# Performance work log

Measured on AMD Instinct MI355X. Metric: run time of the kernel, lower is better.

## Reference

```python
import jax, jax.numpy as jnp
import numpy as np


def setup_inputs() -> dict:
    key = jax.random.key(0)
    k_x, k_q, k_k, k_v = jax.random.split(key, 4)
    B, S, F, U = 8, 2048, 1024, 256
    x = jax.random.normal(k_x, (B, S, F), dtype=jnp.float32)
    Wq = jax.random.normal(k_q, (F, U), dtype=jnp.float32) * 0.05
    Wk = jax.random.normal(k_k, (F, U), dtype=jnp.float32) * 0.05
    Wv = jax.random.normal(k_v, (F, U), dtype=jnp.float32) * 0.05
    return {"x": x, "Wq": Wq, "Wk": Wk, "Wv": Wv}


def reference(x, Wq, Wk, Wv):
    # x: [B, S, F]; projections tanh-activated: [B, S, U]
    xQ = jnp.tanh(jnp.einsum("bsf,fu->bsu", x, Wq))
    xK = jnp.tanh(jnp.einsum("bsf,fu->bsu", x, Wk))
    xV = jnp.tanh(jnp.einsum("bsf,fu->bsu", x, Wv))
    scale = 1.0 / jnp.sqrt(jnp.asarray(x.shape[-1], dtype=jnp.float32))
    scores = jnp.einsum("bsu,btu->bst", xQ, xK) * scale  # [B, S, S]
    weights = jax.nn.softmax(scores, axis=-1)
    out = jnp.einsum("bst,btu->bsu", weights, xV)  # return_sequences=True
    return out
```

## Files before the change

kernel.cpp:

```cpp
#include <hip/hip_runtime.h>
#include <math.h>

#define B_ 8
#define S_ 2048
#define F_ 1024
#define U_ 256
#define M_ (B_ * S_)

typedef __attribute__((ext_vector_type(8))) short bf16x8;
typedef __attribute__((ext_vector_type(4))) float f32x4;
typedef __attribute__((ext_vector_type(16))) float f32x16;
typedef unsigned short ushort_t;

__device__ __forceinline__ unsigned short f2bf(float x) {
    unsigned u = __builtin_bit_cast(unsigned, x);
    unsigned r = (u + 0x7fffu + ((u >> 16) & 1u)) >> 16;
    return (unsigned short)r;
}
__device__ __forceinline__ float bf2f(unsigned short b) {
    return __builtin_bit_cast(float, ((unsigned)b) << 16);
}
__device__ __forceinline__ void gload16(const void* g, void* l) {
    __builtin_amdgcn_global_load_lds(
        (const __attribute__((address_space(1))) unsigned int*)g,
        (__attribute__((address_space(3))) unsigned int*)l, 16, 0, 0);
}
__device__ __forceinline__ f32x4 zero4() {
    f32x4 v; v[0] = 0.f; v[1] = 0.f; v[2] = 0.f; v[3] = 0.f; return v;
}

__global__ __launch_bounds__(256) void convxt_kernel(
    const float* __restrict__ x, ushort_t* __restrict__ xbt)
{
    __shared__ ushort_t T[8][129][8];

    const int t  = threadIdx.x;
    const int r0 = blockIdx.x * 128;
    const int k0 = blockIdx.y * 64;

    #pragma unroll
    for (int i = 0; i < 8; ++i) {
        const int r = i * 16 + (t >> 4);
        const int c = (t & 15) * 4;
        const float4 v = *reinterpret_cast<const float4*>(
            x + (size_t)(r0 + r) * F_ + k0 + c);
        ushort4 o;
        o.x = f2bf(v.x); o.y = f2bf(v.y); o.z = f2bf(v.z); o.w = f2bf(v.w);
        *reinterpret_cast<ushort4*>(&T[c >> 3][r][c & 7]) = o;
    }
    __syncthreads();
    #pragma unroll
    for (int i = 0; i < 4; ++i) {
        const int ci  = i * 256 + t;
        const int ksl = ci >> 7, r = ci & 127;
        ushort_t* dst = xbt + ((size_t)(blockIdx.y * 8 + ksl) * M_ + r0 + r) * 8;
        *reinterpret_cast<bf16x8*>(dst) =
            *reinterpret_cast<const bf16x8*>(&T[ksl][r][0]);
    }
}

__global__ __launch_bounds__(256) void convw_kernel(
    const float* __restrict__ Wq, const float* __restrict__ Wk,
    const float* __restrict__ Wv, ushort_t* __restrict__ Wp)
{
    const int ks   = blockIdx.x;
    const int wsel = blockIdx.y;
    const float* __restrict__ W = (wsel == 0) ? Wq : (wsel == 1) ? Wk : Wv;
    const int n = threadIdx.x;

    bf16x8 hv, lv;
    #pragma unroll
    for (int j = 0; j < 8; ++j) {
        float v = W[(size_t)(ks * 8 + j) * U_ + n];
        ushort_t h = f2bf(v);
        hv[j] = (short)h;
        lv[j] = (short)f2bf(v - bf2f(h));
    }
    size_t base = (size_t)wsel * 524288;
    *reinterpret_cast<bf16x8*>(&Wp[base + ((size_t)ks) * 2048 + n * 8]) = hv;
    *reinterpret_cast<bf16x8*>(&Wp[base + ((size_t)(128 + ks)) * 2048 + n * 8]) = lv;
}

__global__ __launch_bounds__(256, 3) void proj_mfma_kernel(
    const ushort_t* __restrict__ xbt,
    const ushort_t* __restrict__ Wp,
    ushort_t* __restrict__ qh_g, ushort_t* __restrict__ kh_g,
    ushort_t* __restrict__ vth_g)
{
    __shared__ ushort_t As[2][4 * 128 * 8];
    __shared__ ushort_t Bs[2][2 * 4 * 128 * 8];

    const int orig = blockIdx.x;
    const int xcd  = orig & 7;
    const int i    = orig >> 3;
    const int rt6  = i / 6;
    const int sub  = i - rt6 * 6;
    const int wsel = sub >> 1;
    const int nh   = sub & 1;
    const int row0 = (xcd * 16 + rt6) * 128;
    const int col0 = nh * 128;
    const bool twopass = (wsel == 2);

    const int tid = threadIdx.x;
    const int l = tid & 63, w = tid >> 6;
    const int wy = w >> 1, wx = w & 1;
    const int m = l & 31, hi = l >> 5;

    const ushort_t* __restrict__ WpB = Wp + (size_t)wsel * 524288;

    f32x16 acc[2][2];
    #pragma unroll
    for (int mr = 0; mr < 2; ++mr)
        #pragma unroll
        for (int nf = 0; nf < 2; ++nf)
            #pragma unroll
            for (int r = 0; r < 16; ++r) acc[mr][nf][r] = 0.f;

    auto stageA = [&](int buf, int ks) {
        #pragma unroll
        for (int it = 0; it < 2; ++it) {
            const int ci = it * 256 + tid;
            const int ksl = ci >> 7, r = ci & 127;
            const ushort_t* src =
                xbt + ((size_t)(ks * 4 + ksl) * M_ + row0 + r) * 8;
            gload16(src, (char*)&As[buf][0] + (size_t)(it * 256 + w * 64) * 16);
        }
    };
    auto stageB = [&](int buf, int ks) {
        const int nit = twopass ? 4 : 2;
        for (int it = 0; it < nit; ++it) {
            const int ci = it * 256 + tid;
            const int half = ci >> 9, ksl = (ci >> 7) & 3, n = ci & 127;
            const ushort_t* src = WpB + (size_t)half * 262144
                                  + (size_t)(ks * 4 + ksl) * 2048
                                  + (size_t)(col0 + n) * 8;
            gload16(src, (char*)&Bs[buf][0] + (size_t)(it * 256 + w * 64) * 16);
        }
    };

    stageA(0, 0);
    stageB(0, 0);
    __syncthreads();

    for (int ks = 0; ks < 32; ++ks) {
        const int cur = ks & 1;
        if (ks < 31) { stageA(cur ^ 1, ks + 1); stageB(cur ^ 1, ks + 1); }

        const ushort_t* Ac = &As[cur][0];
        const ushort_t* Bc = &Bs[cur][0];

        #pragma unroll
        for (int g = 0; g < 2; ++g) {
            const int ksl = g * 2 + hi;
            bf16x8 ah[2];
            #pragma unroll
            for (int mr = 0; mr < 2; ++mr)
                ah[mr] = *reinterpret_cast<const bf16x8*>(
                    &Ac[(size_t)(ksl * 128 + wy * 64 + mr * 32 + m) * 8]);
            bf16x8 bh[2];
            #pragma unroll
            for (int nf = 0; nf < 2; ++nf) {
                const int nn = wx * 64 + nf * 32 + m;
                bh[nf] = *reinterpret_cast<const bf16x8*>(
                    &Bc[(size_t)(ksl * 128 + nn) * 8]);
            }
            #pragma unroll
            for (int nf = 0; nf < 2; ++nf)
                #pragma unroll
                for (int mr = 0; mr < 2; ++mr)
                    acc[mr][nf] = __builtin_amdgcn_mfma_f32_32x32x16_bf16(
                        ah[mr], bh[nf], acc[mr][nf], 0, 0, 0);
            if (twopass) {
                bf16x8 bl[2];
                #pragma unroll
                for (int nf = 0; nf < 2; ++nf) {
                    const int nn = wx * 64 + nf * 32 + m;
                    bl[nf] = *reinterpret_cast<const bf16x8*>(
                        &Bc[(size_t)(512 * 8 + (ksl * 128 + nn) * 8)]);
                }
                #pragma unroll
                for (int nf = 0; nf < 2; ++nf)
                    #pragma unroll
                    for (int mr = 0; mr < 2; ++mr)
                        acc[mr][nf] = __builtin_amdgcn_mfma_f32_32x32x16_bf16(
                            ah[mr], bl[nf], acc[mr][nf], 0, 0, 0);
            }
        }
        __syncthreads();
    }

    const float oscale = (wsel == 0) ? 0.03125f : 1.0f;
    #pragma unroll
    for (int mr = 0; mr < 2; ++mr) {
        const int row_base = row0 + wy * 64 + mr * 32;
        if (wsel < 2) {
            ushort_t* __restrict__ hp = (wsel == 0) ? qh_g : kh_g;
            #pragma unroll
            for (int nf = 0; nf < 2; ++nf) {
                const int u = col0 + wx * 64 + nf * 32 + m;
                #pragma unroll
                for (int reg = 0; reg < 16; ++reg) {
                    const int rl = (reg & 3) + 8 * (reg >> 2) + 4 * hi;
                    hp[(size_t)(row_base + rl) * U_ + u] =
                        f2bf(tanhf(acc[mr][nf][reg]) * oscale);
                }
            }
        } else {
            const int b     = row0 >> 11;
            const int s_blk = (row0 & 2047) + wy * 64 + mr * 32;
            #pragma unroll
            for (int nf = 0; nf < 2; ++nf) {
                const int u = col0 + wx * 64 + nf * 32 + m;
                #pragma unroll
                for (int rg = 0; rg < 4; ++rg) {
                    ushort4 hv;
                    hv.x = f2bf(tanhf(acc[mr][nf][rg * 4 + 0]));
                    hv.y = f2bf(tanhf(acc[mr][nf][rg * 4 + 1]));
                    hv.z = f2bf(tanhf(acc[mr][nf][rg * 4 + 2]));
                    hv.w = f2bf(tanhf(acc[mr][nf][rg * 4 + 3]));
                    size_t off = ((size_t)b * U_ + u) * S_ + s_blk + 8 * rg + 4 * hi;
                    *reinterpret_cast<ushort4*>(&vth_g[off]) = hv;
                }
            }
        }
    }
}

__global__ __launch_bounds__(256, 2) void attn_mfma_kernel(
    const ushort_t* __restrict__ qh_g,
    const ushort_t* __restrict__ kh_g,
    const ushort_t* __restrict__ vth_g,
    float* __restrict__ O0, float* __restrict__ O1,
    float* __restrict__ ml)
{
    __shared__ ushort_t Kbuf[2][32 * 256];
    __shared__ ushort_t Vbuf[2][256 * 40];
    __shared__ ushort_t Pbuf[4][512];

    const int tid = threadIdx.x;
    const int l  = tid & 63, w = tid >> 6;
    const int kq = l & 15,  g = l >> 4;

    const int logical = (blockIdx.x & 7) * 64 + (blockIdx.x >> 3);
    const int b     = logical >> 6;
    const int qb    = (logical >> 1) & 31;
    const int khalf = logical & 1;
    const int qrow0 = b * S_ + qb * 64 + w * 16;
    const int kb0   = khalf * 1024;

    bf16x8 qh[8];
    {
        const ushort_t* qbh = qh_g + (size_t)(qrow0 + kq) * U_;
        #pragma unroll
        for (int us = 0; us < 8; ++us)
            qh[us] = *reinterpret_cast<const bf16x8*>(qbh + us * 32 + g * 8);
    }

    f32x4 O[16];
    #pragma unroll
    for (int nt = 0; nt < 16; ++nt) O[nt] = zero4();
    float m_run = -INFINITY, l_run = 0.f;

    auto stage = [&](int buf, int k0) {
        #pragma unroll
        for (int i = 0; i < 4; ++i) {
            int c = w * 256 + i * 64 + l;
            int key = c >> 5, uc = c & 31;
            int ucs = uc ^ (key & 7);
            size_t so = (size_t)(b * S_ + k0 + key) * U_ + ucs * 8;
            gload16(kh_g + so, &Kbuf[buf][(w * 256 + i * 64) * 8]);
        }
        #pragma unroll
        for (int i = 0; i < 5; ++i) {
            int c = w * 320 + i * 64 + l;
            int u = (c * 52429) >> 18;
            int kc = c - u * 5;
            size_t so = ((size_t)b * U_ + u) * S_ + k0 + kc * 8;
            const ushort_t* sh = (kc < 4) ? (vth_g + so) : vth_g;
            gload16(sh, &Vbuf[buf][(w * 320 + i * 64) * 8]);
        }
    };

    stage(0, kb0);

    for (int t = 0; t < 32; ++t) {
        const int cur = t & 1;
        asm volatile("s_waitcnt vmcnt(0)" ::: "memory");
        __builtin_amdgcn_s_barrier();
        if (t < 31) stage(cur ^ 1, kb0 + (t + 1) * 32);

        const ushort_t* Kh = Kbuf[cur];
        const ushort_t* Vh = Vbuf[cur];

        f32x4 s0 = zero4(), s1 = zero4();
        #pragma unroll
        for (int us = 0; us < 8; ++us) {
            int off0 = kq * 256 + ((us * 32 + g * 8) ^ ((kq & 7) * 8));
            bf16x8 k0h = *reinterpret_cast<const bf16x8*>(Kh + off0);
            s0 = __builtin_amdgcn_mfma_f32_16x16x32_bf16(k0h, qh[us], s0, 0, 0, 0);
            int off1 = off0 + 16 * 256;
            bf16x8 k1h = *reinterpret_cast<const bf16x8*>(Kh + off1);
            s1 = __builtin_amdgcn_mfma_f32_16x16x32_bf16(k1h, qh[us], s1, 0, 0, 0);
        }

        float tm = fmaxf(fmaxf(fmaxf(s0[0], s0[1]), fmaxf(s0[2], s0[3])),
                         fmaxf(fmaxf(s1[0], s1[1]), fmaxf(s1[2], s1[3])));
        tm = fmaxf(tm, __shfl_xor(tm, 16));
        tm = fmaxf(tm, __shfl_xor(tm, 32));
        const bool defer = __all(tm - m_run <= 4.0f);
        float mn = m_run, f;
        if (!defer) {
            mn = fmaxf(m_run, tm);
            f = __expf(m_run - mn);
            m_run = mn;
        }
        ushort_t ph0[4], ph1[4];
        float su = 0.f;
        #pragma unroll
        for (int r = 0; r < 4; ++r) {
            ph0[r] = f2bf(__expf(s0[r] - mn)); su += bf2f(ph0[r]);
        }
        #pragma unroll
        for (int r = 0; r < 4; ++r) {
            ph1[r] = f2bf(__expf(s1[r] - mn)); su += bf2f(ph1[r]);
        }
        su += __shfl_xor(su, 16);
        su += __shfl_xor(su, 32);

        {
            ushort4 a, c;
            a.x = ph0[0]; a.y = ph0[1]; a.z = ph0[2]; a.w = ph0[3];
            c.x = ph1[0]; c.y = ph1[1]; c.z = ph1[2]; c.w = ph1[3];
            int pw0 = ((g >> 1)) * 128 + kq * 8 + (g & 1) * 4;
            int pw1 = (2 + (g >> 1)) * 128 + kq * 8 + (g & 1) * 4;
            *reinterpret_cast<ushort4*>(&Pbuf[w][pw0]) = a;
            *reinterpret_cast<ushort4*>(&Pbuf[w][pw1]) = c;
        }

        if (defer) {
            l_run += su;
        } else {
            l_run = l_run * f + su;
            float fr0 = __shfl(f, g * 4 + 0), fr1 = __shfl(f, g * 4 + 1);
            float fr2 = __shfl(f, g * 4 + 2), fr3 = __shfl(f, g * 4 + 3);
            #pragma unroll
            for (int nt = 0; nt < 16; ++nt) {
                O[nt][0] *= fr0; O[nt][1] *= fr1;
                O[nt][2] *= fr2; O[nt][3] *= fr3;
            }
        }

        bf16x8 pa_h = *reinterpret_cast<const bf16x8*>(&Pbuf[w][g * 128 + kq * 8]);
        #pragma unroll
        for (int nt = 0; nt < 16; ++nt) {
            int vo = (nt * 16 + kq) * 40 + g * 8;
            bf16x8 vh = *reinterpret_cast<const bf16x8*>(Vh + vo);
            O[nt] = __builtin_amdgcn_mfma_f32_16x16x32_bf16(pa_h, vh, O[nt], 0, 0, 0);
        }
    }

    float* __restrict__ Op = khalf ? O1 : O0;
    #pragma unroll
    for (int nt = 0; nt < 16; ++nt) {
        const int col = nt * 16 + kq;
        Op[(size_t)(qrow0 + g * 4 + 0) * U_ + col] = O[nt][0];
        Op[(size_t)(qrow0 + g * 4 + 1) * U_ + col] = O[nt][1];
        Op[(size_t)(qrow0 + g * 4 + 2) * U_ + col] = O[nt][2];
        Op[(size_t)(qrow0 + g * 4 + 3) * U_ + col] = O[nt][3];
    }
    if (g == 0) {
        ml[((size_t)khalf * M_ + qrow0 + kq) * 2 + 0] = m_run;
        ml[((size_t)khalf * M_ + qrow0 + kq) * 2 + 1] = l_run;
    }
}

__global__ __launch_bounds__(256) void merge_kernel(
    const float* __restrict__ O1, const float* __restrict__ ml,
    float* __restrict__ out)
{
    const int tid = threadIdx.x;
    const int row = blockIdx.x * 4 + (tid >> 6);
    const int c   = (tid & 63) * 4;

    const float m0 = ml[(size_t)row * 2 + 0];
    const float l0 = ml[(size_t)row * 2 + 1];
    const float m1 = ml[((size_t)M_ + row) * 2 + 0];
    const float l1 = ml[((size_t)M_ + row) * 2 + 1];
    const float Mx = fmaxf(m0, m1);
    float a0 = __expf(m0 - Mx), a1 = __expf(m1 - Mx);
    const float inv = 1.f / (a0 * l0 + a1 * l1);
    a0 *= inv; a1 *= inv;

    const size_t off = (size_t)row * U_ + c;
    const float4 o0 = *reinterpret_cast<const float4*>(out + off);
    const float4 o1 = *reinterpret_cast<const float4*>(O1 + off);
    float4 r;
    r.x = o0.x * a0 + o1.x * a1;
    r.y = o0.y * a0 + o1.y * a1;
    r.z = o0.z * a0 + o1.z * a1;
    r.w = o0.w * a0 + o1.w * a1;
    *reinterpret_cast<float4*>(out + off) = r;
}

extern "C" void kernel_launch(void* const* d_in, const int* in_sizes, int n_in,
                              void* d_out, int out_size, void* d_ws, size_t ws_size,
                              hipStream_t stream)
{
    (void)in_sizes; (void)n_in; (void)out_size; (void)ws_size;
    const float* x  = (const float*)d_in[0];
    const float* Wq = (const float*)d_in[1];
    const float* Wk = (const float*)d_in[2];
    const float* Wv = (const float*)d_in[3];
    float* out = (float*)d_out;

    ushort_t* ws = (ushort_t*)d_ws;
    const size_t T = (size_t)M_ * U_;
    ushort_t* qh_g  = ws;
    ushort_t* kh_g  = ws + T;
    ushort_t* vth_g = ws + 2 * T;
    ushort_t* Wp    = ws + 3 * T;
    ushort_t* xbt   = ws + 3 * T + 1572864;
    float*    O1    = (float*)xbt;
    float*    ml    = O1 + T;

    convxt_kernel<<<dim3(128, 16), 256, 0, stream>>>(x, xbt);
    convw_kernel<<<dim3(128, 3), 256, 0, stream>>>(Wq, Wk, Wv, Wp);

    proj_mfma_kernel<<<dim3(768), 256, 0, stream>>>(
        xbt, Wp, qh_g, kh_g, vth_g);

    attn_mfma_kernel<<<dim3(512), 256, 0, stream>>>(
        qh_g, kh_g, vth_g, out, O1, ml);

    merge_kernel<<<dim3(M_ / 4), 256, 0, stream>>>(O1, ml, out);
}
```

Baseline: 146.8 us.

## Read V directly from global memory and split keys four ways for occupancy

The attention kernel no longer stages V tiles in LDS. Each lane loads its V fragments straight from global memory, which frees LDS and lets launch bounds request 4 blocks per CU. When the workspace is large enough, the key range is split into 4 chunks instead of 2, giving twice as many blocks. The merge kernel is generalized to combine nkh partial results. This trades the LDS-cached V reuse for direct global/L2 reads and adds more partial-output traffic in the merge step.

Measured after the change: 251.9 us. 1.72x slower.

```diff
diff --git a/kernel.cpp b/kernel.cpp
--- a/kernel.cpp
+++ b/kernel.cpp
@@ -226,27 +226,29 @@
     }
 }
 
-__global__ __launch_bounds__(256, 2) void attn_mfma_kernel(
+__global__ __launch_bounds__(256, 4) void attn_mfma_kernel(
     const ushort_t* __restrict__ qh_g,
     const ushort_t* __restrict__ kh_g,
     const ushort_t* __restrict__ vth_g,
     float* __restrict__ O0, float* __restrict__ O1,
-    float* __restrict__ ml)
+    float* __restrict__ ml, int nkh)
 {
     __shared__ ushort_t Kbuf[2][32 * 256];
-    __shared__ ushort_t Vbuf[2][256 * 40];
     __shared__ ushort_t Pbuf[4][512];
 
     const int tid = threadIdx.x;
     const int l  = tid & 63, w = tid >> 6;
     const int kq = l & 15,  g = l >> 4;
 
-    const int logical = (blockIdx.x & 7) * 64 + (blockIdx.x >> 3);
-    const int b     = logical >> 6;
-    const int qb    = (logical >> 1) & 31;
-    const int khalf = logical & 1;
-    const int qrow0 = b * S_ + qb * 64 + w * 16;
-    const int kb0   = khalf * 1024;
+    const int per_b = 32 * nkh;
+    const int logical = (blockIdx.x & 7) * per_b + (blockIdx.x >> 3);
+    const int b   = logical / per_b;
+    const int r   = logical - b * per_b;
+    const int qt  = r / nkh;
+    const int kh  = r - qt * nkh;
+    const int ksz = S_ / nkh;
+    const int kb0 = kh * ksz;
+    const int qrow0 = b * S_ + qt * 64 + w * 16;
 
     bf16x8 qh[8];
     {
@@ -261,7 +263,7 @@
     for (int nt = 0; nt < 16; ++nt) O[nt] = zero4();
     float m_run = -INFINITY, l_run = 0.f;
 
-    auto stage = [&](int buf, int k0) {
+    auto stageK = [&](int buf, int k0) {
         #pragma unroll
         for (int i = 0; i < 4; ++i) {
             int c = w * 256 + i * 64 + l;
@@ -270,27 +272,22 @@
             size_t so = (size_t)(b * S_ + k0 + key) * U_ + ucs * 8;
             gload16(kh_g + so, &Kbuf[buf][(w * 256 + i * 64) * 8]);
         }
-        #pragma unroll
-        for (int i = 0; i < 5; ++i) {
-            int c = w * 320 + i * 64 + l;
-            int u = (c * 52429) >> 18;
-            int kc = c - u * 5;
-            size_t so = ((size_t)b * U_ + u) * S_ + k0 + kc * 8;
-            const ushort_t* sh = (kc < 4) ? (vth_g + so) : vth_g;
-            gload16(sh, &Vbuf[buf][(w * 320 + i * 64) * 8]);
-        }
     };
 
-    stage(0, kb0);
-
-    for (int t = 0; t < 32; ++t) {
+    stageK(0, kb0);
+
+    const ushort_t* __restrict__ vrow =
+        vth_g + ((size_t)b * U_ + kq) * S_;
+
+    const int ntile = ksz / 32;
+    for (int t = 0; t < ntile; ++t) {
         const int cur = t & 1;
         asm volatile("s_waitcnt vmcnt(0)" ::: "memory");
         __builtin_amdgcn_s_barrier();
-        if (t < 31) stage(cur ^ 1, kb0 + (t + 1) * 32);
+        if (t < ntile - 1) stageK(cur ^ 1, kb0 + (t + 1) * 32);
 
         const ushort_t* Kh = Kbuf[cur];
-        const ushort_t* Vh = Vbuf[cur];
+        const int key0 = kb0 + t * 32 + g * 8;
 
         f32x4 s0 = zero4(), s1 = zero4();
         #pragma unroll
@@ -317,12 +314,12 @@
         ushort_t ph0[4], ph1[4];
         float su = 0.f;
         #pragma unroll
-        for (int r = 0; r < 4; ++r) {
-            ph0[r] = f2bf(__expf(s0[r] - mn)); su += bf2f(ph0[r]);
-        }
-        #pragma unroll
-        for (int r = 0; r < 4; ++r) {
-            ph1[r] = f2bf(__expf(s1[r] - mn)); su += bf2f(ph1[r]);
+        for (int rr = 0; rr < 4; ++rr) {
+            ph0[rr] = f2bf(__expf(s0[rr] - mn)); su += bf2f(ph0[rr]);
+        }
+        #pragma unroll
+        for (int rr = 0; rr < 4; ++rr) {
+            ph1[rr] = f2bf(__expf(s1[rr] - mn)); su += bf2f(ph1[rr]);
         }
         su += __shfl_xor(su, 16);
         su += __shfl_xor(su, 32);
@@ -353,13 +350,13 @@
         bf16x8 pa_h = *reinterpret_cast<const bf16x8*>(&Pbuf[w][g * 128 + kq * 8]);
         #pragma unroll
         for (int nt = 0; nt < 16; ++nt) {
-            int vo = (nt * 16 + kq) * 40 + g * 8;
-            bf16x8 vh = *reinterpret_cast<const bf16x8*>(Vh + vo);
+            bf16x8 vh = *reinterpret_cast<const bf16x8*>(
+                vrow + (size_t)(nt * 16) * S_ + key0);
             O[nt] = __builtin_amdgcn_mfma_f32_16x16x32_bf16(pa_h, vh, O[nt], 0, 0, 0);
         }
     }
 
-    float* __restrict__ Op = khalf ? O1 : O0;
+    float* __restrict__ Op = (kh == 0) ? O0 : (O1 + (size_t)(kh - 1) * M_ * U_);
     #pragma unroll
     for (int nt = 0; nt < 16; ++nt) {
         const int col = nt * 16 + kq;
@@ -369,44 +366,56 @@
         Op[(size_t)(qrow0 + g * 4 + 3) * U_ + col] = O[nt][3];
     }
     if (g == 0) {
-        ml[((size_t)khalf * M_ + qrow0 + kq) * 2 + 0] = m_run;
-        ml[((size_t)khalf * M_ + qrow0 + kq) * 2 + 1] = l_run;
+        ml[((size_t)kh * M_ + qrow0 + kq) * 2 + 0] = m_run;
+        ml[((size_t)kh * M_ + qrow0 + kq) * 2 + 1] = l_run;
     }
 }
 
 __global__ __launch_bounds__(256) void merge_kernel(
     const float* __restrict__ O1, const float* __restrict__ ml,
-    float* __restrict__ out)
+    float* __restrict__ out, int nkh)
 {
     const int tid = threadIdx.x;
     const int row = blockIdx.x * 4 + (tid >> 6);
     const int c   = (tid & 63) * 4;
 
-    const float m0 = ml[(size_t)row * 2 + 0];
-    const float l0 = ml[(size_t)row * 2 + 1];
-    const float m1 = ml[((size_t)M_ + row) * 2 + 0];
-    const float l1 = ml[((size_t)M_ + row) * 2 + 1];
-    const float Mx = fmaxf(m0, m1);
-    float a0 = __expf(m0 - Mx), a1 = __expf(m1 - Mx);
-    const float inv = 1.f / (a0 * l0 + a1 * l1);
-    a0 *= inv; a1 *= inv;
+    float mv[4], lv[4];
+    float Mx = -INFINITY;
+    for (int j = 0; j < nkh; ++j) {
+        mv[j] = ml[((size_t)j * M_ + row) * 2 + 0];
+        lv[j] = ml[((size_t)j * M_ + row) * 2 + 1];
+        Mx = fmaxf(Mx, mv[j]);
+    }
+    float denom = 0.f;
+    float a[4];
+    for (int j = 0; j < nkh; ++j) {
+        a[j] = __expf(mv[j] - Mx);
+        denom += a[j] * lv[j];
+    }
+    const float inv = 1.f / denom;
 
     const size_t off = (size_t)row * U_ + c;
-    const float4 o0 = *reinterpret_cast<const float4*>(out + off);
-    const float4 o1 = *reinterpret_cast<const float4*>(O1 + off);
-    float4 r;
-    r.x = o0.x * a0 + o1.x * a1;
-    r.y = o0.y * a0 + o1.y * a1;
-    r.z = o0.z * a0 + o1.z * a1;
-    r.w = o0.w * a0 + o1.w * a1;
-    *reinterpret_cast<float4*>(out + off) = r;
+    float4 racc;
+    {
+        const float4 o0 = *reinterpret_cast<const float4*>(out + off);
+        const float s = a[0] * inv;
+        racc.x = o0.x * s; racc.y = o0.y * s; racc.z = o0.z * s; racc.w = o0.w * s;
+    }
+    for (int j = 1; j < nkh; ++j) {
+        const float4 oj = *reinterpret_cast<const float4*>(
+            O1 + (size_t)(j - 1) * M_ * U_ + off);
+        const float s = a[j] * inv;
+        racc.x += oj.x * s; racc.y += oj.y * s;
+        racc.z += oj.z * s; racc.w += oj.w * s;
+    }
+    *reinterpret_cast<float4*>(out + off) = racc;
 }
 
 extern "C" void kernel_launch(void* const* d_in, const int* in_sizes, int n_in,
                               void* d_out, int out_size, void* d_ws, size_t ws_size,
                               hipStream_t stream)
 {
-    (void)in_sizes; (void)n_in; (void)out_size; (void)ws_size;
+    (void)in_sizes; (void)n_in; (void)out_size;
     const float* x  = (const float*)d_in[0];
     const float* Wq = (const float*)d_in[1];
     const float* Wk = (const float*)d_in[2];
@@ -421,7 +430,8 @@
     ushort_t* Wp    = ws + 3 * T;
     ushort_t* xbt   = ws + 3 * T + 1572864;
     float*    O1    = (float*)xbt;
-    float*    ml    = O1 + T;
+    const int nkh   = (ws_size >= 79167488ull) ? 4 : 2;
+    float*    ml    = O1 + (size_t)(nkh - 1) * T;
 
     convxt_kernel<<<dim3(128, 16), 256, 0, stream>>>(x, xbt);
     convw_kernel<<<dim3(128, 3), 256, 0, stream>>>(Wq, Wk, Wv, Wp);
@@ -429,8 +439,8 @@
     proj_mfma_kernel<<<dim3(768), 256, 0, stream>>>(
         xbt, Wp, qh_g, kh_g, vth_g);
 
-    attn_mfma_kernel<<<dim3(512), 256, 0, stream>>>(
-        qh_g, kh_g, vth_g, out, O1, ml);
-
-    merge_kernel<<<dim3(M_ / 4), 256, 0, stream>>>(O1, ml, out);
-}
+    attn_mfma_kernel<<<dim3(256 * nkh), 256, 0, stream>>>(
+        qh_g, kh_g, vth_g, out, O1, ml, nkh);
+
+    merge_kernel<<<dim3(M_ / 4), 256, 0, stream>>>(O1, ml, out, nkh);
+}
```
